# Optimization experiments

Hardware: AMD Instinct MI355X
Metric: run time of the kernel (lower is better)

Reference implementation:

```python
import jax, jax.numpy as jnp
import numpy as np

B, R, A, V, L = 256, 512, 196, 10000, 2
I = R  # input_size == rnn_size (required for stacked layers)


def setup_inputs() -> dict:
    key = jax.random.key(0)
    ks = jax.random.split(key, 18)
    s = 0.05
    return {
        "x": jax.random.normal(ks[0], (B, I), jnp.float32),
        "att": jax.random.normal(ks[1], (B, A, R), jnp.float32),
        "inputs": jax.random.normal(ks[2], (2 * L, B, R), jnp.float32),
        "Wa2a": jax.random.normal(ks[3], (A, R), jnp.float32) * s,
        "ba2a": jnp.zeros((A,), jnp.float32),
        "Wh2a": jax.random.normal(ks[4], (A, R), jnp.float32) * s,
        "bh2a": jnp.zeros((A,), jnp.float32),
        "wd2d": jax.random.normal(ks[5], (A,), jnp.float32) * s,
        "bd2d": jnp.zeros((1,), jnp.float32),
        "Wi2h": jax.random.normal(ks[6], (4 * R, I), jnp.float32) * s,
        "bi2h": jnp.zeros((4 * R,), jnp.float32),
        "Wh2h": jax.random.normal(ks[7], (4 * R, R), jnp.float32) * s,
        "bh2h": jnp.zeros((4 * R,), jnp.float32),
        "Wr2a": jax.random.normal(ks[8], (4 * R, R), jnp.float32) * s,
        "br2a": jnp.zeros((4 * R,), jnp.float32),
        "Wproj": jax.random.normal(ks[9], (V, R), jnp.float32) * s,
        "bproj": jnp.zeros((V,), jnp.float32),
    }


def reference(x, att, inputs, Wa2a, ba2a, Wh2a, bh2a, wd2d, bd2d,
              Wi2h, bi2h, Wh2h, bh2h, Wr2a, br2a, Wproj, bproj):
    # att: [B, A, R]  (A spatial positions, R features); inputs: [2L, B, R]
    states = []
    cur = x
    # a2a(att) is layer-independent but the original recomputes it; einsum below
    # is cheap so we keep the per-layer structure faithful & simple.
    for i in range(L):
        prev_c = inputs[2 * i]
        prev_h = inputs[2 * i + 1]
        # attention scoring: att_v[b,i,a] + att_h[b,i] (unsqueeze(2).expand)
        att_v = jnp.einsum('bir,ar->bia', att, Wa2a) + ba2a          # [B,A,A]
        att_h = prev_h @ Wh2a.T + bh2a                               # [B,A]
        dot = jnp.tanh(att_v + att_h[:, :, None])                    # [B,A,A]
        score = jnp.einsum('bia,a->bi', dot, wd2d) + bd2d            # [B,A]
        w = jax.nn.softmax(score, axis=-1)                           # [B,A]
        att_res = jnp.einsum('bir,bi->br', att, w)                   # [B,R]
        sums = (cur @ Wi2h.T + bi2h) + (prev_h @ Wh2h.T + bh2h) + (att_res @ Wr2a.T + br2a)
        gates = jax.nn.sigmoid(sums[:, :3 * R])
        in_gate = gates[:, :R]
        forget_gate = gates[:, R:2 * R]
        out_gate = gates[:, 2 * R:3 * R]
        in_transform = jnp.tanh(sums[:, 3 * R:])
        next_c = forget_gate * prev_c + in_gate * in_transform
        next_h = out_gate * jnp.tanh(next_c)
        states.append(next_c)
        states.append(next_h)
        cur = next_h
    logsoft = jax.nn.log_softmax(cur @ Wproj.T + bproj, axis=-1)     # [B,V]
    return jnp.stack(states), logsoft
```

## Files before the change

kernel.cpp:

```cpp
#include <hip/hip_runtime.h>
#include <hip/hip_bf16.h>
#include <cstdint>
#include <cstddef>

#define BB 256
#define RR 512
#define AA 196
#define VV 10000
#define MATT (BB*AA)
#define NT13 13

typedef float f32x4 __attribute__((ext_vector_type(4)));
typedef __bf16 bf16x8 __attribute__((ext_vector_type(8)));
typedef __bf16 bf16x4 __attribute__((ext_vector_type(4)));

#define MFMA16(a,b,c) __builtin_amdgcn_mfma_f32_16x16x32_bf16(a,b,c,0,0,0)

__device__ __forceinline__ float fast_tanh(float x){
  float ax = fabsf(x);
  float e = __expf(-2.0f*ax);
  float t = __fdividef(1.0f - e, 1.0f + e);
  return x < 0.0f ? -t : t;
}

__device__ __forceinline__ void gload16(const void* gsrc, void* ldsdst){
  __builtin_amdgcn_global_load_lds(
      (const __attribute__((address_space(1))) unsigned int*)gsrc,
      (__attribute__((address_space(3))) unsigned int*)ldsdst,
      16, 0, 0);
}

#define ABAR   asm volatile("s_barrier" ::: "memory")
#define WVM(N) asm volatile("s_waitcnt vmcnt(" #N ")" ::: "memory")

#define CVT8(a, f0, f1) do { \
  a[0]=(__bf16)(f0).x; a[1]=(__bf16)(f0).y; a[2]=(__bf16)(f0).z; a[3]=(__bf16)(f0).w; \
  a[4]=(__bf16)(f1).x; a[5]=(__bf16)(f1).y; a[6]=(__bf16)(f1).z; a[7]=(__bf16)(f1).w; \
} while(0)

__global__ void cvt4_k(const float* __restrict__ src, __bf16* __restrict__ dst, int n4){
  int i = blockIdx.x*256 + threadIdx.x;
  if (i < n4){
    float4 v = ((const float4*)src)[i];
    bf16x4 o;
    o[0]=(__bf16)v.x; o[1]=(__bf16)v.y; o[2]=(__bf16)v.z; o[3]=(__bf16)v.w;
    ((bf16x4*)dst)[i] = o;
  }
}

__global__ void cvt_padrows_k(const float* __restrict__ src, __bf16* __restrict__ dst, int nvalid){
  int i = blockIdx.x*256 + threadIdx.x;
  int row = i >> 9;
  dst[i] = (__bf16)((row < nvalid) ? src[(size_t)row*512 + (i & 511)] : 0.0f);
}

__global__ void wcat2_k(const float* __restrict__ Wi2h, const float* __restrict__ Wh2h,
                        const float* __restrict__ Wr2a, __bf16* __restrict__ Wcat){
  int k = blockIdx.x*256 + threadIdx.x;
  int n = blockIdx.y;
  float v;
  if (k < 512)       v = Wi2h[n*512 + k];
  else if (k < 1024) v = Wh2h[n*512 + (k-512)];
  else               v = Wr2a[n*512 + (k-1024)];
  Wcat[(size_t)n*1536 + k] = (__bf16)v;
}

__global__ void build_small_k(const float* __restrict__ ba2a, const float* __restrict__ wd2d,
                              const float* __restrict__ bi2h, const float* __restrict__ bh2h,
                              const float* __restrict__ br2a,
                              float* __restrict__ ba_pad, float* __restrict__ wd_pad,
                              float* __restrict__ bcat){
  int i = blockIdx.x*256 + threadIdx.x;
  if (i < 2048){
    bcat[i] = bi2h[i] + bh2h[i] + br2a[i];
  } else if (i < 2048+208){
    int j = i - 2048; ba_pad[j] = (j < AA) ? ba2a[j] : 0.0f;
  } else if (i < 2048+416){
    int j = i - 2256; wd_pad[j] = (j < AA) ? wd2d[j] : 0.0f;
  }
}

__global__ __launch_bounds__(256,4) void gemm3_k(
    const __bf16* __restrict__ A, const __bf16* __restrict__ Bw,
    const float* __restrict__ bias, float* __restrict__ C,
    int N, int K, int NC)
{
  __shared__ __bf16 AshAll[3*2048];
  __shared__ __bf16 BshAll[3*4096];
  const int t = threadIdx.x;
  const int l = t & 63;
  const int w = t >> 6;
  const int l15 = l & 15;
  const int g  = l >> 4;
  const int rho = l15 & 7;
  const int mrow = blockIdx.y*32;
  const int ncb  = blockIdx.x*64;

  const int arow = t >> 3, aj = t & 7;
  const __bf16* as_ = A + (size_t)(mrow + arow)*K + ((aj ^ (arow&7)) << 3);
  const int aoff = w*512;
  const __bf16* bs0_ = Bw + (size_t)(ncb + arow)*K      + ((aj ^ (arow&7)) << 3);
  const __bf16* bs1_ = Bw + (size_t)(ncb + 32 + arow)*K + ((aj ^ (arow&7)) << 3);
  const int boff0 = w*512;
  const int boff1 = 2048 + w*512;

#define G3_STAGE(B, CH) do { \
    gload16(as_  + (CH)*64, AshAll + (B)*2048 + aoff); \
    gload16(bs0_ + (CH)*64, BshAll + (B)*4096 + boff0); \
    gload16(bs1_ + (CH)*64, BshAll + (B)*4096 + boff1); \
  } while(0)

  f32x4 acc0 = {}, acc1 = {};

#define G3_COMPUTE(B) do { \
    const __bf16* As_ = AshAll + (B)*2048; \
    const __bf16* Bs_ = BshAll + (B)*4096; \
    _Pragma("unroll") \
    for (int s_ = 0; s_ < 2; s_++){ \
      int q_ = (((s_<<2)+g) ^ rho) << 3; \
      bf16x8 a0_ = *(const bf16x8*)(As_ + l15*64 + q_); \
      bf16x8 a1_ = *(const bf16x8*)(As_ + (l15+16)*64 + q_); \
      bf16x8 b_  = *(const bf16x8*)(Bs_ + (w*16+l15)*64 + q_); \
      acc0 = MFMA16(a0_, b_, acc0); \
      acc1 = MFMA16(a1_, b_, acc1); \
    } \
  } while(0)

  G3_STAGE(0,0); G3_STAGE(1,1); G3_STAGE(2,2);
  WVM(6); ABAR;
  int buf = 0;
  for (int c = 0; c < NC; c++){
    G3_COMPUTE(buf);
    if (c + 3 < NC){
      ABAR;
      G3_STAGE(buf, c+3);
      WVM(6); ABAR;
    } else if (c == NC-3){
      WVM(3); ABAR;
    } else if (c == NC-2){
      WVM(0); ABAR;
    }
    buf = (buf == 2) ? 0 : buf + 1;
  }

  int col = ncb + w*16 + l15;
  if (col < N){
    float bv = bias[col];
    #pragma unroll
    for (int r = 0; r < 4; r++){
      C[(size_t)(mrow + g*4 + r)*N + col]      = acc0[r] + bv;
      C[(size_t)(mrow + 16 + g*4 + r)*N + col] = acc1[r] + bv;
    }
  }
#undef G3_STAGE
#undef G3_COMPUTE
}

__global__ __launch_bounds__(256,2) void att_score5_k(
    const float* __restrict__ att, const __bf16* __restrict__ Wa2a_p,
    const float* __restrict__ ba_pad, const float* __restrict__ wd_pad,
    const float* __restrict__ att_h, float* __restrict__ score)
{
  __shared__ __bf16 Bsh[3*13312];
  const int t = threadIdx.x;
  const int l = t & 63;
  const int w = t >> 6;
  const int l15 = l & 15;
  const int g  = l >> 4;
  const int rho = l15 & 7;
  const int rowbase = blockIdx.x * 64;

  const __bf16* bsrc[7]; int bslot[7];
  #pragma unroll
  for (int i = 0; i < 7; i++){
    int id = i*4 + w;
    if (id >= 26) id -= 2;
    int slotbase = id*64;
    int slot = slotbase + l;
    int row = slot >> 3;
    int j   = slot & 7;
    bslot[i] = slotbase*8;
    bsrc[i]  = Wa2a_p + (size_t)row*RR + ((j ^ (row&7))<<3);
  }

  const float* pa = att + (size_t)(rowbase + w*16 + l15)*RR + g*8;

  f32x4 acc[NT13] = {};
  float4 p00,p01,p02,p03, p10,p11,p12,p13, p20,p21,p22,p23;

#define SC_STAGE(B, KC) do { \
    _Pragma("unroll") \
    for (int i_ = 0; i_ < 7; i_++) gload16(bsrc[i_] + (KC), Bsh + (B)*13312 + bslot[i_]); \
  } while(0)
#define SC_LOADA(S, KC) do { \
    p##S##0 = *(const float4*)(pa + (KC)); \
    p##S##1 = *(const float4*)(pa + (KC) + 4); \
    p##S##2 = *(const float4*)(pa + (KC) + 32); \
    p##S##3 = *(const float4*)(pa + (KC) + 36); \
  } while(0)
#define SC_COMPUTE(B, S) do { \
    { bf16x8 a_; CVT8(a_, p##S##0, p##S##1); \
      const int sw_ = (g ^ rho) << 3; \
      _Pragma("unroll") \
      for (int nt_ = 0; nt_ < NT13; nt_++){ \
        bf16x8 b_ = *(const bf16x8*)&Bsh[(B)*13312 + nt_*1024 + l15*64 + sw_]; \
        acc[nt_] = MFMA16(a_, b_, acc[nt_]); } } \
    { bf16x8 a_; CVT8(a_, p##S##2, p##S##3); \
      const int sw_ = ((4 + g) ^ rho) << 3; \
      _Pragma("unroll") \
      for (int nt_ = 0; nt_ < NT13; nt_++){ \
        bf16x8 b_ = *(const bf16x8*)&Bsh[(B)*13312 + nt_*1024 + l15*64 + sw_]; \
        acc[nt_] = MFMA16(a_, b_, acc[nt_]); } } \
  } while(0)

  SC_STAGE(0,0);   SC_LOADA(0,0);
  SC_STAGE(1,64);  SC_LOADA(1,64);
  SC_STAGE(2,128); SC_LOADA(2,128);
  WVM(22); ABAR;
  SC_COMPUTE(0,0); ABAR; SC_STAGE(0,192); SC_LOADA(0,192); WVM(22); ABAR;
  SC_COMPUTE(1,1); ABAR; SC_STAGE(1,256); SC_LOADA(1,256); WVM(22); ABAR;
  SC_COMPUTE(2,2); ABAR; SC_STAGE(2,320); SC_LOADA(2,320); WVM(22); ABAR;
  SC_COMPUTE(0,0); ABAR; SC_STAGE(0,384); SC_LOADA(0,384); WVM(22); ABAR;
  SC_COMPUTE(1,1); ABAR; SC_STAGE(1,448); SC_LOADA(1,448); WVM(22); ABAR;
  SC_COMPUTE(2,2); WVM(11); ABAR;
  SC_COMPUTE(0,0); WVM(0);  ABAR;
  SC_COMPUTE(1,1);

  float wdv[NT13], bav[NT13];
  #pragma unroll
  for (int nt = 0; nt < NT13; nt++){
    int col = nt*16 + l15;
    wdv[nt] = wd_pad[col];
    bav[nt] = ba_pad[col];
  }
  #pragma unroll
  for (int r = 0; r < 4; r++){
    int row = rowbase + w*16 + g*4 + r;
    float ah0 = att_h[row];
    float ah1 = att_h[MATT + row];
    float s0 = 0.0f, s1 = 0.0f;
    #pragma unroll
    for (int nt = 0; nt < NT13; nt++){
      float v = acc[nt][r] + bav[nt];
      s0 += fast_tanh(v + ah0) * wdv[nt];
      s1 += fast_tanh(v + ah1) * wdv[nt];
    }
    #pragma unroll
    for (int o = 1; o < 16; o <<= 1){
      s0 += __shfl_xor(s0, o, 16);
      s1 += __shfl_xor(s1, o, 16);
    }
    if (l15 == 0){
      score[row] = s0;
      score[MATT + row] = s1;
    }
  }
#undef SC_STAGE
#undef SC_LOADA
#undef SC_COMPUTE
}

__global__ void softmax196_k(const float* __restrict__ score, float* __restrict__ wsm){
  int lb = blockIdx.x;
  int t = threadIdx.x;
  const float* s = score + (size_t)lb*AA;
  float v0 = (t      < AA) ? s[t]       : -3.4e38f;
  float v1 = (t+64   < AA) ? s[t+64]    : -3.4e38f;
  float v2 = (t+128  < AA) ? s[t+128]   : -3.4e38f;
  float v3 = (t+192  < AA) ? s[t+192]   : -3.4e38f;
  float mx = fmaxf(fmaxf(v0,v1), fmaxf(v2,v3));
  #pragma unroll
  for (int o = 1; o < 64; o <<= 1) mx = fmaxf(mx, __shfl_xor(mx, o, 64));
  float e0 = (t      < AA) ? __expf(v0 - mx) : 0.0f;
  float e1 = (t+64   < AA) ? __expf(v1 - mx) : 0.0f;
  float e2 = (t+128  < AA) ? __expf(v2 - mx) : 0.0f;
  float e3 = (t+192  < AA) ? __expf(v3 - mx) : 0.0f;
  float sum = e0+e1+e2+e3;
  #pragma unroll
  for (int o = 1; o < 64; o <<= 1) sum += __shfl_xor(sum, o, 64);
  float inv = 1.0f / sum;
  float* o_ = wsm + (size_t)lb*AA;
  if (t      < AA) o_[t]     = e0*inv;
  if (t+64   < AA) o_[t+64]  = e1*inv;
  if (t+128  < AA) o_[t+128] = e2*inv;
  if (t+192  < AA) o_[t+192] = e3*inv;
}

__global__ __launch_bounds__(512) void attres3_k(
    const float* __restrict__ att, const float* __restrict__ wsm,
    const float* __restrict__ x, const float* __restrict__ inputs,
    __bf16* __restrict__ Xcat0, __bf16* __restrict__ Xcat1){
  int b = blockIdx.x, t = threadIdx.x;
  __shared__ float w0[208], w1[208];
  __shared__ float4 redv[4][128];
  if (t < AA) w0[t] = wsm[(size_t)b*AA + t];
  int t2 = t - 256;
  if (t2 >= 0 && t2 < AA) w1[t2] = wsm[(size_t)(256+b)*AA + t2];
  Xcat0[(size_t)b*1536 + t]       = (__bf16)x[(size_t)b*512 + t];
  Xcat0[(size_t)b*1536 + 512 + t] = (__bf16)inputs[(size_t)1*131072 + b*512 + t];
  Xcat1[(size_t)b*1536 + 512 + t] = (__bf16)inputs[(size_t)3*131072 + b*512 + t];
  __syncthreads();
  int cg = t & 127, ig = t >> 7;
  const float4* ap = (const float4*)(att + (size_t)b*AA*RR) + cg;
  float4 s0 = {0,0,0,0}, s1 = {0,0,0,0};
  #pragma unroll 4
  for (int i = ig; i < AA; i += 4){
    float4 v = ap[(size_t)i*128];
    float a0 = w0[i], a1 = w1[i];
    s0.x += v.x*a0; s0.y += v.y*a0; s0.z += v.z*a0; s0.w += v.w*a0;
    s1.x += v.x*a1; s1.y += v.y*a1; s1.z += v.z*a1; s1.w += v.w*a1;
  }
  redv[ig][cg] = s0; __syncthreads();
  if (t < 128){
    float4 a = redv[0][t], b4 = redv[1][t], c4 = redv[2][t], d4 = redv[3][t];
    __bf16* o = Xcat0 + (size_t)b*1536 + 1024 + t*4;
    o[0]=(__bf16)(a.x+b4.x+c4.x+d4.x); o[1]=(__bf16)(a.y+b4.y+c4.y+d4.y);
    o[2]=(__bf16)(a.z+b4.z+c4.z+d4.z); o[3]=(__bf16)(a.w+b4.w+c4.w+d4.w);
  }
  __syncthreads();
  redv[ig][cg] = s1; __syncthreads();
  if (t < 128){
    float4 a = redv[0][t], b4 = redv[1][t], c4 = redv[2][t], d4 = redv[3][t];
    __bf16* o = Xcat1 + (size_t)b*1536 + 1024 + t*4;
    o[0]=(__bf16)(a.x+b4.x+c4.x+d4.x); o[1]=(__bf16)(a.y+b4.y+c4.y+d4.y);
    o[2]=(__bf16)(a.z+b4.z+c4.z+d4.z); o[3]=(__bf16)(a.w+b4.w+c4.w+d4.w);
  }
}

__global__ void gate_k(const float* __restrict__ sums, const float* __restrict__ prev_c,
                       float* __restrict__ out_c, float* __restrict__ out_h,
                       __bf16* __restrict__ hdst, int hstride){
  int idx = blockIdx.x*256 + threadIdx.x;
  int b = idx >> 9, r = idx & 511;
  const float* s = sums + (size_t)b*2048;
  float ig = 1.0f/(1.0f + __expf(-s[r]));
  float fg = 1.0f/(1.0f + __expf(-s[512+r]));
  float og = 1.0f/(1.0f + __expf(-s[1024+r]));
  float g  = fast_tanh(s[1536+r]);
  float c = fg*prev_c[idx] + ig*g;
  float h = og*fast_tanh(c);
  out_c[idx] = c;
  out_h[idx] = h;
  hdst[(size_t)b*hstride + r] = (__bf16)h;
}

__global__ void logsoftmax_k(const float* __restrict__ logits, float* __restrict__ out){
  int b = blockIdx.x, t = threadIdx.x;
  __shared__ float red[4], red2[4];
  const float* p = logits + (size_t)b*VV;
  float mx = -3.4e38f;
  for (int i = t; i < VV; i += 256) mx = fmaxf(mx, p[i]);
  #pragma unroll
  for (int o = 1; o < 64; o <<= 1) mx = fmaxf(mx, __shfl_xor(mx, o, 64));
  if ((t & 63) == 0) red[t >> 6] = mx;
  __syncthreads();
  mx = fmaxf(fmaxf(red[0], red[1]), fmaxf(red[2], red[3]));
  float sum = 0.0f;
  for (int i = t; i < VV; i += 256) sum += __expf(p[i] - mx);
  #pragma unroll
  for (int o = 1; o < 64; o <<= 1) sum += __shfl_xor(sum, o, 64);
  if ((t & 63) == 0) red2[t >> 6] = sum;
  __syncthreads();
  sum = red2[0] + red2[1] + red2[2] + red2[3];
  float lse = mx + logf(sum);
  float* q = out + (size_t)b*VV;
  for (int i = t; i < VV; i += 256) q[i] = p[i] - lse;
}

extern "C" void kernel_launch(void* const* d_in, const int* in_sizes, int n_in,
                              void* d_out_, int out_size, void* d_ws, size_t ws_size,
                              hipStream_t stream){
  const float* x     = (const float*)d_in[0];
  const float* att   = (const float*)d_in[1];
  const float* inputs= (const float*)d_in[2];
  const float* Wa2a  = (const float*)d_in[3];
  const float* ba2a  = (const float*)d_in[4];
  const float* Wh2a  = (const float*)d_in[5];
  const float* bh2a  = (const float*)d_in[6];
  const float* wd2d  = (const float*)d_in[7];
  const float* Wi2h  = (const float*)d_in[9];
  const float* bi2h  = (const float*)d_in[10];
  const float* Wh2h  = (const float*)d_in[11];
  const float* bh2h  = (const float*)d_in[12];
  const float* Wr2a  = (const float*)d_in[13];
  const float* br2a  = (const float*)d_in[14];
  const float* Wproj = (const float*)d_in[15];
  const float* bproj = (const float*)d_in[16];
  float* d_out = (float*)d_out_;

  char* wsp = (char*)d_ws;
  auto alloc = [&](size_t bytes)->char*{
    char* p = wsp;
    wsp += (bytes + 255) & ~(size_t)255;
    return p;
  };
  __bf16* Wa2a_p   = (__bf16*)alloc((size_t)208*RR*2);
  __bf16* Wh2a_pad = (__bf16*)alloc((size_t)256*RR*2);
  __bf16* Wcat_bf  = (__bf16*)alloc((size_t)2048*1536*2);
  __bf16* Wproj_bf = (__bf16*)alloc((size_t)10048*RR*2);
  __bf16* inp_bf   = (__bf16*)alloc((size_t)512*RR*2);
  float* ba_pad = (float*)alloc(208*4);
  float* wd_pad = (float*)alloc(208*4);
  float* bcat   = (float*)alloc(2048*4);
  float* att_h  = (float*)alloc((size_t)2*MATT*4);
  float* score  = (float*)alloc((size_t)2*MATT*4);
  float* wsm    = (float*)alloc((size_t)2*MATT*4);
  __bf16* Xcat0 = (__bf16*)alloc((size_t)BB*1536*2);
  __bf16* Xcat1 = (__bf16*)alloc((size_t)BB*1536*2);
  float* sums   = (float*)alloc((size_t)BB*2048*4);
  __bf16* h1_bf = (__bf16*)alloc((size_t)BB*RR*2);
  float* logits = (float*)alloc((size_t)BB*VV*4);

  cvt_padrows_k<<<(208*512)/256, 256, 0, stream>>>(Wa2a, Wa2a_p, AA);
  cvt_padrows_k<<<(256*512)/256, 256, 0, stream>>>(Wh2a, Wh2a_pad, AA);
  cvt_padrows_k<<<(10048*512)/256, 256, 0, stream>>>(Wproj, Wproj_bf, VV);
  cvt4_k<<<(131072/4)/256, 256, 0, stream>>>(inputs + 1*131072, inp_bf, 131072/4);
  cvt4_k<<<(131072/4)/256, 256, 0, stream>>>(inputs + 3*131072, inp_bf + 131072, 131072/4);
  wcat2_k<<<dim3(6,2048), 256, 0, stream>>>(Wi2h, Wh2h, Wr2a, Wcat_bf);
  build_small_k<<<10, 256, 0, stream>>>(ba2a, wd2d, bi2h, bh2h, br2a, ba_pad, wd_pad, bcat);

  gemm3_k<<<dim3(4,16), 256, 0, stream>>>(inp_bf, Wh2a_pad, bh2a, att_h, AA, 512, 8);
  att_score5_k<<<784, 256, 0, stream>>>(att, Wa2a_p, ba_pad, wd_pad, att_h, score);
  softmax196_k<<<512, 64, 0, stream>>>(score, wsm);
  attres3_k<<<256, 512, 0, stream>>>(att, wsm, x, inputs, Xcat0, Xcat1);

  gemm3_k<<<dim3(32,8), 256, 0, stream>>>(Xcat0, Wcat_bf, bcat, sums, 2048, 1536, 24);
  gate_k<<<512, 256, 0, stream>>>(sums, inputs, d_out, d_out + 131072, Xcat1, 1536);
  gemm3_k<<<dim3(32,8), 256, 0, stream>>>(Xcat1, Wcat_bf, bcat, sums, 2048, 1536, 24);
  gate_k<<<512, 256, 0, stream>>>(sums, inputs + 2*131072, d_out + 2*131072, d_out + 3*131072, h1_bf, 512);

  gemm3_k<<<dim3(157,8), 256, 0, stream>>>(h1_bf, Wproj_bf, bproj, logits, VV, 512, 8);
  logsoftmax_k<<<256, 256, 0, stream>>>(logits, d_out + 4*131072);
}
```

Baseline: 166.5 us.

## Restructure attention-score pipeline with smaller K chunks and vectorize conversion kernels

The attention score kernel now streams K in 16 chunks of 32 with a triple-buffered 16KB LDS B tile, allowing three blocks per CU. It staggers each block's starting chunk to spread L2 traffic and remaps block-to-tile order. Weight conversion, concat, attres stores and log-softmax are vectorized to float4/bf16x4 accesses to cut instruction and memory-transaction overhead. Padding buffers grow to 256 rows to match the new staging layout. The smaller chunks add more barriers per block.

```diff
diff --git a/kernel.cpp b/kernel.cpp
--- a/kernel.cpp
+++ b/kernel.cpp
@@ -48,21 +48,27 @@
   }
 }
 
-__global__ void cvt_padrows_k(const float* __restrict__ src, __bf16* __restrict__ dst, int nvalid){
-  int i = blockIdx.x*256 + threadIdx.x;
-  int row = i >> 9;
-  dst[i] = (__bf16)((row < nvalid) ? src[(size_t)row*512 + (i & 511)] : 0.0f);
-}
-
-__global__ void wcat2_k(const float* __restrict__ Wi2h, const float* __restrict__ Wh2h,
+__global__ void cvt_padrows4_k(const float* __restrict__ src, __bf16* __restrict__ dst, int nvalid){
+  int i4 = blockIdx.x*256 + threadIdx.x;
+  int row = i4 >> 7, k4 = i4 & 127;
+  float4 v = {0,0,0,0};
+  if (row < nvalid) v = ((const float4*)(src + (size_t)row*512))[k4];
+  bf16x4 o;
+  o[0]=(__bf16)v.x; o[1]=(__bf16)v.y; o[2]=(__bf16)v.z; o[3]=(__bf16)v.w;
+  ((bf16x4*)(dst))[i4] = o;
+}
+
+__global__ void wcat4_k(const float* __restrict__ Wi2h, const float* __restrict__ Wh2h,
                         const float* __restrict__ Wr2a, __bf16* __restrict__ Wcat){
-  int k = blockIdx.x*256 + threadIdx.x;
-  int n = blockIdx.y;
-  float v;
-  if (k < 512)       v = Wi2h[n*512 + k];
-  else if (k < 1024) v = Wh2h[n*512 + (k-512)];
-  else               v = Wr2a[n*512 + (k-1024)];
-  Wcat[(size_t)n*1536 + k] = (__bf16)v;
+  int k4 = threadIdx.x;
+  int n  = blockIdx.x;
+  float4 v;
+  if (k4 < 128)      v = ((const float4*)(Wi2h + (size_t)n*512))[k4];
+  else if (k4 < 256) v = ((const float4*)(Wh2h + (size_t)n*512))[k4-128];
+  else               v = ((const float4*)(Wr2a + (size_t)n*512))[k4-256];
+  bf16x4 o;
+  o[0]=(__bf16)v.x; o[1]=(__bf16)v.y; o[2]=(__bf16)v.z; o[3]=(__bf16)v.w;
+  ((bf16x4*)(Wcat + (size_t)n*1536))[k4] = o;
 }
 
 __global__ void build_small_k(const float* __restrict__ ba2a, const float* __restrict__ wd2d,
@@ -73,10 +79,10 @@
   int i = blockIdx.x*256 + threadIdx.x;
   if (i < 2048){
     bcat[i] = bi2h[i] + bh2h[i] + br2a[i];
-  } else if (i < 2048+208){
+  } else if (i < 2048+256){
     int j = i - 2048; ba_pad[j] = (j < AA) ? ba2a[j] : 0.0f;
-  } else if (i < 2048+416){
-    int j = i - 2256; wd_pad[j] = (j < AA) ? wd2d[j] : 0.0f;
+  } else if (i < 2048+512){
+    int j = i - 2304; wd_pad[j] = (j < AA) ? wd2d[j] : 0.0f;
   }
 }
 
@@ -156,75 +162,78 @@
 #undef G3_COMPUTE
 }
 
-__global__ __launch_bounds__(256,2) void att_score5_k(
+__global__ __launch_bounds__(256,3) void att_score8_k(
     const float* __restrict__ att, const __bf16* __restrict__ Wa2a_p,
     const float* __restrict__ ba_pad, const float* __restrict__ wd_pad,
     const float* __restrict__ att_h, float* __restrict__ score)
 {
-  __shared__ __bf16 Bsh[3*13312];
+  __shared__ __bf16 Bsh[3*8192];
   const int t = threadIdx.x;
   const int l = t & 63;
   const int w = t >> 6;
-  const int l15 = l & 15;
-  const int g  = l >> 4;
-  const int rho = l15 & 7;
-  const int rowbase = blockIdx.x * 64;
-
-  const __bf16* bsrc[7]; int bslot[7];
-  #pragma unroll
-  for (int i = 0; i < 7; i++){
-    int id = i*4 + w;
-    if (id >= 26) id -= 2;
-    int slotbase = id*64;
-    int slot = slotbase + l;
-    int row = slot >> 3;
-    int j   = slot & 7;
-    bslot[i] = slotbase*8;
-    bsrc[i]  = Wa2a_p + (size_t)row*RR + ((j ^ (row&7))<<3);
+  const int l15 = l & 15, g = l >> 4;
+
+  const int bid = blockIdx.x;
+  const int tile = (bid & 7) * 98 + (bid >> 3);
+  const int rowbase = tile * 64;
+  const int phase = bid & 15;
+
+  const __bf16* bsrc[4]; int boff[4];
+  #pragma unroll
+  for (int i = 0; i < 4; i++){
+    int slot = i*256 + t;
+    int row = slot >> 2, j2 = slot & 3;
+    boff[i] = (i*256 + (t & ~63)) * 8;
+    bsrc[i] = Wa2a_p + (size_t)row*RR + ((j2 ^ (row&3)) << 3);
   }
 
   const float* pa = att + (size_t)(rowbase + w*16 + l15)*RR + g*8;
 
   f32x4 acc[NT13] = {};
-  float4 p00,p01,p02,p03, p10,p11,p12,p13, p20,p21,p22,p23;
-
-#define SC_STAGE(B, KC) do { \
+  float4 a00,a01, a10,a11, a20,a21;
+
+#define S8_STAGE(BUF, CH) do { \
+    int kc_ = (CH)*32; \
+    gload16(bsrc[0] + kc_, Bsh + (BUF)*8192 + boff[0]); \
+    gload16(bsrc[1] + kc_, Bsh + (BUF)*8192 + boff[1]); \
+    gload16(bsrc[2] + kc_, Bsh + (BUF)*8192 + boff[2]); \
+    gload16(bsrc[3] + kc_, Bsh + (BUF)*8192 + boff[3]); \
+  } while(0)
+#define S8_LOADA(S, CH) do { \
+    a##S##0 = *(const float4*)(pa + (CH)*32); \
+    a##S##1 = *(const float4*)(pa + (CH)*32 + 4); \
+  } while(0)
+#define S8_COMPUTE(BUF, S) do { \
+    bf16x8 a_; CVT8(a_, a##S##0, a##S##1); \
+    const __bf16* Bs_ = Bsh + (BUF)*8192; \
     _Pragma("unroll") \
-    for (int i_ = 0; i_ < 7; i_++) gload16(bsrc[i_] + (KC), Bsh + (B)*13312 + bslot[i_]); \
-  } while(0)
-#define SC_LOADA(S, KC) do { \
-    p##S##0 = *(const float4*)(pa + (KC)); \
-    p##S##1 = *(const float4*)(pa + (KC) + 4); \
-    p##S##2 = *(const float4*)(pa + (KC) + 32); \
-    p##S##3 = *(const float4*)(pa + (KC) + 36); \
-  } while(0)
-#define SC_COMPUTE(B, S) do { \
-    { bf16x8 a_; CVT8(a_, p##S##0, p##S##1); \
-      const int sw_ = (g ^ rho) << 3; \
-      _Pragma("unroll") \
-      for (int nt_ = 0; nt_ < NT13; nt_++){ \
-        bf16x8 b_ = *(const bf16x8*)&Bsh[(B)*13312 + nt_*1024 + l15*64 + sw_]; \
-        acc[nt_] = MFMA16(a_, b_, acc[nt_]); } } \
-    { bf16x8 a_; CVT8(a_, p##S##2, p##S##3); \
-      const int sw_ = ((4 + g) ^ rho) << 3; \
-      _Pragma("unroll") \
-      for (int nt_ = 0; nt_ < NT13; nt_++){ \
-        bf16x8 b_ = *(const bf16x8*)&Bsh[(B)*13312 + nt_*1024 + l15*64 + sw_]; \
-        acc[nt_] = MFMA16(a_, b_, acc[nt_]); } } \
-  } while(0)
-
-  SC_STAGE(0,0);   SC_LOADA(0,0);
-  SC_STAGE(1,64);  SC_LOADA(1,64);
-  SC_STAGE(2,128); SC_LOADA(2,128);
-  WVM(22); ABAR;
-  SC_COMPUTE(0,0); ABAR; SC_STAGE(0,192); SC_LOADA(0,192); WVM(22); ABAR;
-  SC_COMPUTE(1,1); ABAR; SC_STAGE(1,256); SC_LOADA(1,256); WVM(22); ABAR;
-  SC_COMPUTE(2,2); ABAR; SC_STAGE(2,320); SC_LOADA(2,320); WVM(22); ABAR;
-  SC_COMPUTE(0,0); ABAR; SC_STAGE(0,384); SC_LOADA(0,384); WVM(22); ABAR;
-  SC_COMPUTE(1,1); ABAR; SC_STAGE(1,448); SC_LOADA(1,448); WVM(22); ABAR;
-  SC_COMPUTE(2,2); WVM(11); ABAR;
-  SC_COMPUTE(0,0); WVM(0);  ABAR;
-  SC_COMPUTE(1,1);
+    for (int nt_ = 0; nt_ < NT13; nt_++){ \
+      int br_ = nt_*16 + l15; \
+      bf16x8 b_ = *(const bf16x8*)(Bs_ + br_*32 + ((g ^ (br_&3))<<3)); \
+      acc[nt_] = MFMA16(a_, b_, acc[nt_]); \
+    } \
+  } while(0)
+#define CH(i) (((i) + phase) & 15)
+
+  S8_STAGE(0, CH(0)); S8_LOADA(0, CH(0));
+  S8_STAGE(1, CH(1)); S8_LOADA(1, CH(1));
+  S8_STAGE(2, CH(2)); S8_LOADA(2, CH(2));
+  WVM(12); ABAR;
+
+#define S8_ITER(c, S) do { \
+    S8_COMPUTE(S, S); \
+    if ((c) < 13){ \
+      ABAR; \
+      S8_STAGE(S, CH((c)+3)); S8_LOADA(S, CH((c)+3)); \
+      WVM(12); ABAR; \
+    } else if ((c) == 13){ WVM(6); ABAR; } \
+    else if ((c) == 14){ WVM(0); ABAR; } \
+  } while(0)
+
+  S8_ITER(0,0);  S8_ITER(1,1);  S8_ITER(2,2);  S8_ITER(3,0);
+  S8_ITER(4,1);  S8_ITER(5,2);  S8_ITER(6,0);  S8_ITER(7,1);
+  S8_ITER(8,2);  S8_ITER(9,0);  S8_ITER(10,1); S8_ITER(11,2);
+  S8_ITER(12,0); S8_ITER(13,1); S8_ITER(14,2); S8_ITER(15,0);
 
   float wdv[NT13], bav[NT13];
   #pragma unroll
@@ -255,9 +264,11 @@
       score[MATT + row] = s1;
     }
   }
-#undef SC_STAGE
-#undef SC_LOADA
-#undef SC_COMPUTE
+#undef S8_STAGE
+#undef S8_LOADA
+#undef S8_COMPUTE
+#undef S8_ITER
+#undef CH
 }
 
 __global__ void softmax196_k(const float* __restrict__ score, float* __restrict__ wsm){
@@ -313,17 +324,19 @@
   redv[ig][cg] = s0; __syncthreads();
   if (t < 128){
     float4 a = redv[0][t], b4 = redv[1][t], c4 = redv[2][t], d4 = redv[3][t];
-    __bf16* o = Xcat0 + (size_t)b*1536 + 1024 + t*4;
+    bf16x4 o;
     o[0]=(__bf16)(a.x+b4.x+c4.x+d4.x); o[1]=(__bf16)(a.y+b4.y+c4.y+d4.y);
     o[2]=(__bf16)(a.z+b4.z+c4.z+d4.z); o[3]=(__bf16)(a.w+b4.w+c4.w+d4.w);
+    *(bf16x4*)(Xcat0 + (size_t)b*1536 + 1024 + t*4) = o;
   }
   __syncthreads();
   redv[ig][cg] = s1; __syncthreads();
   if (t < 128){
     float4 a = redv[0][t], b4 = redv[1][t], c4 = redv[2][t], d4 = redv[3][t];
-    __bf16* o = Xcat1 + (size_t)b*1536 + 1024 + t*4;
+    bf16x4 o;
     o[0]=(__bf16)(a.x+b4.x+c4.x+d4.x); o[1]=(__bf16)(a.y+b4.y+c4.y+d4.y);
     o[2]=(__bf16)(a.z+b4.z+c4.z+d4.z); o[3]=(__bf16)(a.w+b4.w+c4.w+d4.w);
+    *(bf16x4*)(Xcat1 + (size_t)b*1536 + 1024 + t*4) = o;
   }
 }
 
@@ -344,27 +357,37 @@
   hdst[(size_t)b*hstride + r] = (__bf16)h;
 }
 
-__global__ void logsoftmax_k(const float* __restrict__ logits, float* __restrict__ out){
+__global__ void logsoftmax4_k(const float* __restrict__ logits, float* __restrict__ out){
   int b = blockIdx.x, t = threadIdx.x;
   __shared__ float red[4], red2[4];
-  const float* p = logits + (size_t)b*VV;
+  const float4* p = (const float4*)(logits + (size_t)b*VV);
   float mx = -3.4e38f;
-  for (int i = t; i < VV; i += 256) mx = fmaxf(mx, p[i]);
+  for (int i = t; i < 2500; i += 256){
+    float4 v = p[i];
+    mx = fmaxf(mx, fmaxf(fmaxf(v.x,v.y), fmaxf(v.z,v.w)));
+  }
   #pragma unroll
   for (int o = 1; o < 64; o <<= 1) mx = fmaxf(mx, __shfl_xor(mx, o, 64));
   if ((t & 63) == 0) red[t >> 6] = mx;
   __syncthreads();
   mx = fmaxf(fmaxf(red[0], red[1]), fmaxf(red[2], red[3]));
   float sum = 0.0f;
-  for (int i = t; i < VV; i += 256) sum += __expf(p[i] - mx);
+  for (int i = t; i < 2500; i += 256){
+    float4 v = p[i];
+    sum += __expf(v.x-mx) + __expf(v.y-mx) + __expf(v.z-mx) + __expf(v.w-mx);
+  }
   #pragma unroll
   for (int o = 1; o < 64; o <<= 1) sum += __shfl_xor(sum, o, 64);
   if ((t & 63) == 0) red2[t >> 6] = sum;
   __syncthreads();
   sum = red2[0] + red2[1] + red2[2] + red2[3];
   float lse = mx + logf(sum);
-  float* q = out + (size_t)b*VV;
-  for (int i = t; i < VV; i += 256) q[i] = p[i] - lse;
+  float4* q = (float4*)(out + (size_t)b*VV);
+  for (int i = t; i < 2500; i += 256){
+    float4 v = p[i];
+    v.x -= lse; v.y -= lse; v.z -= lse; v.w -= lse;
+    q[i] = v;
+  }
 }
 
 extern "C" void kernel_launch(void* const* d_in, const int* in_sizes, int n_in,
@@ -394,13 +417,13 @@
     wsp += (bytes + 255) & ~(size_t)255;
     return p;
   };
-  __bf16* Wa2a_p   = (__bf16*)alloc((size_t)208*RR*2);
+  __bf16* Wa2a_p   = (__bf16*)alloc((size_t)256*RR*2);
   __bf16* Wh2a_pad = (__bf16*)alloc((size_t)256*RR*2);
   __bf16* Wcat_bf  = (__bf16*)alloc((size_t)2048*1536*2);
   __bf16* Wproj_bf = (__bf16*)alloc((size_t)10048*RR*2);
   __bf16* inp_bf   = (__bf16*)alloc((size_t)512*RR*2);
-  float* ba_pad = (float*)alloc(208*4);
-  float* wd_pad = (float*)alloc(208*4);
+  float* ba_pad = (float*)alloc(256*4);
+  float* wd_pad = (float*)alloc(256*4);
   float* bcat   = (float*)alloc(2048*4);
   float* att_h  = (float*)alloc((size_t)2*MATT*4);
   float* score  = (float*)alloc((size_t)2*MATT*4);
@@ -411,16 +434,17 @@
   __bf16* h1_bf = (__bf16*)alloc((size_t)BB*RR*2);
   float* logits = (float*)alloc((size_t)BB*VV*4);
 
-  cvt_padrows_k<<<(208*512)/256, 256, 0, stream>>>(Wa2a, Wa2a_p, AA);
-  cvt_padrows_k<<<(256*512)/256, 256, 0, stream>>>(Wh2a, Wh2a_pad, AA);
-  cvt_padrows_k<<<(10048*512)/256, 256, 0, stream>>>(Wproj, Wproj_bf, VV);
+  cvt_padrows4_k<<<(256*128)/256, 256, 0, stream>>>(Wa2a, Wa2a_p, AA);
+  cvt_padrows4_k<<<(256*128)/256, 256, 0, stream>>>(Wh2a, Wh2a_pad, AA);
+  cvt_padrows4_k<<<(10048*128)/256, 256, 0, stream>>>(Wproj, Wproj_bf, VV);
   cvt4_k<<<(131072/4)/256, 256, 0, stream>>>(inputs + 1*131072, inp_bf, 131072/4);
   cvt4_k<<<(131072/4)/256, 256, 0, stream>>>(inputs + 3*131072, inp_bf + 131072, 131072/4);
-  wcat2_k<<<dim3(6,2048), 256, 0, stream>>>(Wi2h, Wh2h, Wr2a, Wcat_bf);
+  wcat4_k<<<2048, 384, 0, stream>>>(Wi2h, Wh2h, Wr2a, Wcat_bf);
   build_small_k<<<10, 256, 0, stream>>>(ba2a, wd2d, bi2h, bh2h, br2a, ba_pad, wd_pad, bcat);
 
   gemm3_k<<<dim3(4,16), 256, 0, stream>>>(inp_bf, Wh2a_pad, bh2a, att_h, AA, 512, 8);
-  att_score5_k<<<784, 256, 0, stream>>>(att, Wa2a_p, ba_pad, wd_pad, att_h, score);
+
+  att_score8_k<<<784, 256, 0, stream>>>(att, Wa2a_p, ba_pad, wd_pad, att_h, score);
   softmax196_k<<<512, 64, 0, stream>>>(score, wsm);
   attres3_k<<<256, 512, 0, stream>>>(att, wsm, x, inputs, Xcat0, Xcat1);
 
@@ -430,5 +454,5 @@
   gate_k<<<512, 256, 0, stream>>>(sums, inputs + 2*131072, d_out + 2*131072, d_out + 3*131072, h1_bf, 512);
 
   gemm3_k<<<dim3(157,8), 256, 0, stream>>>(h1_bf, Wproj_bf, bproj, logits, VV, 512, 8);
-  logsoftmax_k<<<256, 256, 0, stream>>>(logits, d_out + 4*131072);
-}
+  logsoftmax4_k<<<256, 256, 0, stream>>>(logits, d_out + 4*131072);
+}
```

After: 160.4 us. 3.7% less time.
